# Optimization experiments

Measured on AMD Instinct MI355X. Metric: run time of the kernel, lower is better.

## Reference

```python
import jax, jax.numpy as jnp
import numpy as np
import math

NUM_HEADS = 32
KV_HEADS = 8
HEAD_DIM = 64
ROPE_BASE = 10000.0


def rotate_half(x):
    x1, x2 = jnp.split(x, 2, axis=-1)
    return jnp.concatenate([-x2, x1], axis=-1)


def rope_cos_sin(seq_len, head_dim, dtype):
    inv_freq = 1.0 / (ROPE_BASE ** (jnp.arange(0, head_dim, 2, dtype=jnp.float32) / head_dim))
    pos = jnp.arange(seq_len, dtype=jnp.float32)
    freqs = pos[:, None] * inv_freq[None, :]          # [S, D/2]
    emb = jnp.concatenate([freqs, freqs], axis=-1)    # [S, D]
    return jnp.cos(emb).astype(dtype), jnp.sin(emb).astype(dtype)


def setup_inputs() -> dict:
    key = jax.random.key(0)
    k1, k2, k3, k4, k5 = jax.random.split(key, 5)
    B, S, H = 2, 2048, 2048
    sc = 1.0 / math.sqrt(H)
    return {
        "hidden_states": jax.random.normal(k1, (B, S, H), jnp.float32),
        "Wq": jax.random.normal(k2, (H, H), jnp.float32) * sc,
        "Wk": jax.random.normal(k3, (KV_HEADS * HEAD_DIM, H), jnp.float32) * sc,
        "Wv": jax.random.normal(k4, (KV_HEADS * HEAD_DIM, H), jnp.float32) * sc,
        "Wo": jax.random.normal(k5, (H, H), jnp.float32) * sc,
    }


def reference(hidden_states, Wq, Wk, Wv, Wo):
    B, S, H = hidden_states.shape
    # projections (torch Linear: x @ W.T)
    q = (hidden_states @ Wq.T).reshape(B, S, NUM_HEADS, HEAD_DIM).transpose(0, 2, 1, 3)   # [B,Hq,S,D]
    k = (hidden_states @ Wk.T).reshape(B, S, KV_HEADS, HEAD_DIM).transpose(0, 2, 1, 3)    # [B,Hk,S,D]
    v = (hidden_states @ Wv.T).reshape(B, S, KV_HEADS, HEAD_DIM).transpose(0, 2, 1, 3)
    # inline RoPE
    cos, sin = rope_cos_sin(S, HEAD_DIM, q.dtype)   # [S,D], broadcasts over [B,h,S,D]
    q = q * cos + rotate_half(q) * sin
    k = k * cos + rotate_half(k) * sin
    # GQA: repeat KV heads
    rep = NUM_HEADS // KV_HEADS
    k = jnp.repeat(k, rep, axis=1)
    v = jnp.repeat(v, rep, axis=1)
    # scores + causal mask + softmax
    scores = jnp.einsum('bhqd,bhkd->bhqk', q, k) / math.sqrt(HEAD_DIM)
    causal = jnp.tril(jnp.ones((S, S), dtype=bool))
    scores = jnp.where(causal[None, None], scores, jnp.float32(-1e9))
    probs = jax.nn.softmax(scores.astype(jnp.float32), axis=-1).astype(q.dtype)
    ctx = jnp.einsum('bhqk,bhkd->bhqd', probs, v)
    ctx = ctx.transpose(0, 2, 1, 3).reshape(B, S, NUM_HEADS * HEAD_DIM)
    return ctx @ Wo.T
```

## Files before the change

### kernel.cpp

```cpp
#include <hip/hip_runtime.h>
#include <cstdint>
#include <cstddef>

typedef unsigned short ushort_t;
typedef __bf16 bf16x8 __attribute__((ext_vector_type(8)));
typedef ushort_t us8 __attribute__((ext_vector_type(8)));
typedef float f32x4 __attribute__((ext_vector_type(4)));

__device__ __forceinline__ ushort_t f2bf(float f) {
  union { float f; uint32_t u; } x; x.f = f;
  uint32_t r = (x.u + 0x7fffu + ((x.u >> 16) & 1u)) >> 16;
  return (ushort_t)r;
}
__device__ __forceinline__ float bf2f(ushort_t u) {
  union { uint32_t u; float f; } x; x.u = ((uint32_t)u) << 16;
  return x.f;
}
__device__ __forceinline__ float exp2_hw(float x) {
  float r;
  asm volatile("v_exp_f32 %0, %1\n\ts_nop 0" : "=v"(r) : "v"(x));
  return r;
}
__device__ __forceinline__ void gload_lds16(const void* g, void* l) {
  __builtin_amdgcn_global_load_lds(
      (const __attribute__((address_space(1))) void*)g,
      (__attribute__((address_space(3))) void*)l, 16, 0, 0);
}

__global__ void f32_to_bf16_kn(const float* __restrict__ in,
                               ushort_t* __restrict__ out, int n) {
  int i = (blockIdx.x * blockDim.x + threadIdx.x) * 4;
  if (i >= n) return;
  float4 v = *(const float4*)(in + i);
  ushort4 o;
  o.x = f2bf(v.x); o.y = f2bf(v.y); o.z = f2bf(v.z); o.w = f2bf(v.w);
  *(ushort4*)(out + i) = o;
}

__global__ void wconvert_kn(const float* __restrict__ Wq, const float* __restrict__ Wk,
                            const float* __restrict__ Wv, const float* __restrict__ Wo,
                            ushort_t* __restrict__ out) {
  int i = (blockIdx.x * blockDim.x + threadIdx.x) * 4;
  const float* src;
  int off;
  if (i < 4194304)      { src = Wq; off = i; }
  else if (i < 5242880) { src = Wk; off = i - 4194304; }
  else if (i < 6291456) { src = Wv; off = i - 5242880; }
  else                  { src = Wo; off = i - 6291456; }
  float4 v = *(const float4*)(src + off);
  ushort4 o;
  o.x = f2bf(v.x); o.y = f2bf(v.y); o.z = f2bf(v.z); o.w = f2bf(v.w);
  *(ushort4*)(out + i) = o;
}

template <int OUT_MODE>
__global__ __launch_bounds__(256, 2) void gemm_bt(
    const ushort_t* __restrict__ A, const ushort_t* __restrict__ Bw,
    void* __restrict__ Cout, void* __restrict__ Cout2, int M, int N, int K) {
  __shared__ __align__(16) ushort_t As[128 * 32];
  __shared__ __align__(16) ushort_t Bs[128 * 32];
  const int tid = threadIdx.x;
  const int lane = tid & 63;
  const int l15 = lane & 15, lq = lane >> 4;
  const int wid = tid >> 6;
  const int wm = (wid >> 1) * 64, wn = (wid & 1) * 64;
  const int m0 = blockIdx.x * 128, n0 = blockIdx.y * 128;

  const int seg = tid & 3;
  const int rrow = tid >> 2;
  const size_t aBase = (size_t)m0 * K + seg * 8;
  const size_t bBase = (size_t)n0 * K + seg * 8;
  const int ldsWaveBase = (tid & ~63) * 16;

  f32x4 acc[4][4] = {};
  const int nkt = K >> 5;
  for (int kt = 0; kt < nkt; ++kt) {
    const int kOff = kt * 32;
    __syncthreads();
#pragma unroll
    for (int j = 0; j < 2; ++j) {
      int row = j * 64 + rrow;
      gload_lds16(A + aBase + (size_t)row * K + kOff,
                  (char*)As + j * 4096 + ldsWaveBase);
      gload_lds16(Bw + bBase + (size_t)row * K + kOff,
                  (char*)Bs + j * 4096 + ldsWaveBase);
    }
    __syncthreads();
    bf16x8 af[4], bfv[4];
#pragma unroll
    for (int i = 0; i < 4; ++i) {
      af[i]  = *(const bf16x8*)(As + (wm + i * 16 + l15) * 32 + lq * 8);
      bfv[i] = *(const bf16x8*)(Bs + (wn + i * 16 + l15) * 32 + lq * 8);
    }
#pragma unroll
    for (int i = 0; i < 4; ++i)
#pragma unroll
      for (int j = 0; j < 4; ++j)
        acc[i][j] = __builtin_amdgcn_mfma_f32_16x16x32_bf16(af[i], bfv[j],
                                                            acc[i][j], 0, 0, 0);
  }

  if (OUT_MODE == 1) {
    float* C = (float*)Cout;
#pragma unroll
    for (int i = 0; i < 4; ++i) {
      int row = m0 + wm + i * 16 + lq * 4;
#pragma unroll
      for (int j = 0; j < 4; ++j) {
        int col = n0 + wn + j * 16 + l15;
#pragma unroll
        for (int r = 0; r < 4; ++r)
          C[(size_t)(row + r) * N + col] = acc[i][j][r];
      }
    }
  } else {
    ushort_t* qr = (ushort_t*)Cout;
    ushort_t* kvr = (ushort_t*)Cout2;
#pragma unroll
    for (int i = 0; i < 4; ++i) {
      int row = m0 + wm + i * 16 + lq * 4;
#pragma unroll
      for (int j = 0; j < 4; ++j) {
        int col = n0 + wn + j * 16 + l15;
#pragma unroll
        for (int r = 0; r < 4; ++r) {
          int rr = row + r;
          int b = rr >> 11, s = rr & 2047;
          if (col < 2048) {
            int h = col >> 6, d = col & 63;
            qr[((size_t)(b * 32 + h) * 2048 + s) * 64 + d] = f2bf(acc[i][j][r]);
          } else {
            int n2 = col - 2048;
            int head = n2 >> 6, d = n2 & 63;
            kvr[((size_t)(b * 16 + head) * 2048 + s) * 64 + d] = f2bf(acc[i][j][r]);
          }
        }
      }
    }
  }
}

__global__ void rope_kn(ushort_t* __restrict__ X, int nh, int batch_stride,
                        float scale, int total) {
  int idx = blockIdx.x * blockDim.x + threadIdx.x;
  if (idx >= total) return;
  int p = idx & 31;
  int t = idx >> 5;
  int s = t & 2047;
  int bh = t >> 11;
  int h = bh % nh, b = bh / nh;
  ushort_t* row = X + (size_t)b * batch_stride + ((size_t)h * 2048 + s) * 64;
  float a = (float)s * __builtin_exp2f((float)p * -0.4152410118609203f);
  float sn, c;
  __sincosf(a, &sn, &c);
  float x0 = bf2f(row[p]), x1 = bf2f(row[p + 32]);
  row[p]      = f2bf((x0 * c - x1 * sn) * scale);
  row[p + 32] = f2bf((x1 * c + x0 * sn) * scale);
}

#define PAD_K 72
#define PAD_P 76
__global__ __launch_bounds__(256, 4) void attn_kn(
    const ushort_t* __restrict__ Q, const ushort_t* __restrict__ KV,
    ushort_t* __restrict__ ctx) {
  __shared__ __align__(16) ushort_t Ks[64 * PAD_K];
  __shared__ __align__(16) ushort_t Vs[80 * PAD_K];
  __shared__ __align__(16) ushort_t Ps[4][16 * PAD_P];
  const int tid = threadIdx.x, wid = tid >> 6, lane = tid & 63;
  const int l15 = lane & 15, lq = lane >> 4;
  const int g = blockIdx.x;
  const int bh = g & 63;
  const int qidx = g >> 6;
  const int jq = qidx >> 2, sl = qidx & 3;
  const int qb = (jq & 1) ? (12 - 4 * jq + sl) : (15 - 4 * jq - sl);
  const int b = bh >> 5, h = bh & 31, hk = h >> 2;
  const int q0 = qb * 128;
  const int wq0 = q0 + wid * 32;

  for (int i = tid; i < 16 * PAD_K; i += 256)
    Vs[64 * PAD_K + i] = (i < PAD_K) ? (ushort_t)0x3F80 : (ushort_t)0;

  const ushort_t* Qb = Q + ((size_t)(b * 32 + h) * 2048) * 64;
  const ushort_t* Kb = KV + ((size_t)(b * 16 + hk) * 2048) * 64;
  const ushort_t* Vb = KV + ((size_t)(b * 16 + 8 + hk) * 2048) * 64;

  bf16x8 qf[2][2];
#pragma unroll
  for (int qg = 0; qg < 2; ++qg)
#pragma unroll
    for (int ks = 0; ks < 2; ++ks)
      qf[qg][ks] = *(const bf16x8*)(Qb + (size_t)(wq0 + qg * 16 + l15) * 64 +
                                    ks * 32 + lq * 8);

  f32x4 acc[2][5] = {};

  const int srow = tid >> 3, sseg = tid & 7;
  const int vd = tid & 63, vkg = tid >> 6;

  const int nkt = 2 * qb + 2;
  us8 kr0, kr1, vr0, vr1;
  {
    kr0 = *(const us8*)(Kb + (size_t)srow * 64 + sseg * 8);
    kr1 = *(const us8*)(Kb + (size_t)(32 + srow) * 64 + sseg * 8);
#pragma unroll
    for (int i = 0; i < 8; ++i) vr0[i] = Vb[(size_t)(vkg * 16 + i) * 64 + vd];
#pragma unroll
    for (int i = 0; i < 8; ++i) vr1[i] = Vb[(size_t)(vkg * 16 + 8 + i) * 64 + vd];
  }

  for (int kt = 0; kt < nkt; ++kt) {
    const int k0 = kt * 64;
    __syncthreads();
    *(us8*)(Ks + srow * PAD_K + sseg * 8) = kr0;
    *(us8*)(Ks + (32 + srow) * PAD_K + sseg * 8) = kr1;
    *(us8*)(Vs + vd * PAD_K + vkg * 16) = vr0;
    *(us8*)(Vs + vd * PAD_K + vkg * 16 + 8) = vr1;
    if (kt + 1 < nkt) {
      const int k1 = k0 + 64;
      kr0 = *(const us8*)(Kb + (size_t)(k1 + srow) * 64 + sseg * 8);
      kr1 = *(const us8*)(Kb + (size_t)(k1 + 32 + srow) * 64 + sseg * 8);
#pragma unroll
      for (int i = 0; i < 8; ++i)
        vr0[i] = Vb[(size_t)(k1 + vkg * 16 + i) * 64 + vd];
#pragma unroll
      for (int i = 0; i < 8; ++i)
        vr1[i] = Vb[(size_t)(k1 + vkg * 16 + 8 + i) * 64 + vd];
    }
    __syncthreads();

    if (k0 > wq0 + 31) continue;

#pragma unroll
    for (int qg = 0; qg < 2; ++qg) {
      const int rq0 = wq0 + qg * 16;
      f32x4 sf[4] = {};
      __builtin_amdgcn_s_setprio(1);
#pragma unroll
      for (int j = 0; j < 4; ++j)
#pragma unroll
        for (int ks = 0; ks < 2; ++ks)
          sf[j] = __builtin_amdgcn_mfma_f32_16x16x32_bf16(
              qf[qg][ks],
              *(const bf16x8*)(Ks + (j * 16 + l15) * PAD_K + ks * 32 + lq * 8),
              sf[j], 0, 0, 0);
      __builtin_amdgcn_s_setprio(0);

      if (k0 + 63 > rq0) {
#pragma unroll
        for (int j = 0; j < 4; ++j) {
          int kg = k0 + j * 16 + l15;
#pragma unroll
          for (int r = 0; r < 4; ++r) {
            int qrow = rq0 + lq * 4 + r;
            float p = (kg > qrow) ? 0.0f : exp2_hw(sf[j][r]);
            Ps[wid][(lq * 4 + r) * PAD_P + j * 16 + l15] = f2bf(p);
          }
        }
      } else {
#pragma unroll
        for (int j = 0; j < 4; ++j)
#pragma unroll
          for (int r = 0; r < 4; ++r)
            Ps[wid][(lq * 4 + r) * PAD_P + j * 16 + l15] = f2bf(exp2_hw(sf[j][r]));
      }

      bf16x8 pa[2];
#pragma unroll
      for (int ks = 0; ks < 2; ++ks)
        pa[ks] = *(const bf16x8*)(Ps[wid] + l15 * PAD_P + ks * 32 + lq * 8);

      __builtin_amdgcn_s_setprio(1);
#pragma unroll
      for (int dj = 0; dj < 5; ++dj) {
#pragma unroll
        for (int ks = 0; ks < 2; ++ks)
          acc[qg][dj] = __builtin_amdgcn_mfma_f32_16x16x32_bf16(
              pa[ks],
              *(const bf16x8*)(Vs + (dj * 16 + l15) * PAD_K + ks * 32 + lq * 8),
              acc[qg][dj], 0, 0, 0);
      }
      __builtin_amdgcn_s_setprio(0);
    }
  }

#pragma unroll
  for (int qg = 0; qg < 2; ++qg) {
    float linv[4];
#pragma unroll
    for (int r = 0; r < 4; ++r)
      linv[r] = 1.0f / __shfl(acc[qg][4][r], lane & 48);
#pragma unroll
    for (int dj = 0; dj < 4; ++dj)
#pragma unroll
      for (int r = 0; r < 4; ++r) {
        int qrow = wq0 + qg * 16 + lq * 4 + r;
        ctx[((size_t)(b * 2048 + qrow)) * 2048 + h * 64 + dj * 16 + l15] =
            f2bf(acc[qg][dj][r] * linv[r]);
      }
  }
}

extern "C" void kernel_launch(void* const* d_in, const int* in_sizes, int n_in,
                              void* d_out, int out_size, void* d_ws, size_t ws_size,
                              hipStream_t stream) {
  const float* hs = (const float*)d_in[0];
  const float* Wq = (const float*)d_in[1];
  const float* Wk = (const float*)d_in[2];
  const float* Wv = (const float*)d_in[3];
  const float* Wo = (const float*)d_in[4];

  char* ws = (char*)d_ws;
  ushort_t* hb   = (ushort_t*)(ws);
  ushort_t* wqb  = (ushort_t*)(ws + 16777216);
  ushort_t* wob  = (ushort_t*)(ws + 29360128);
  ushort_t* qr   = (ushort_t*)(ws + 37748736);
  ushort_t* kvr  = (ushort_t*)(ws + 54525952);
  ushort_t* ctx  = hb;

  f32_to_bf16_kn<<<8192, 256, 0, stream>>>(hs, hb, 8388608);
  wconvert_kn<<<10240, 256, 0, stream>>>(Wq, Wk, Wv, Wo, wqb);

  gemm_bt<2><<<dim3(32, 24), 256, 0, stream>>>(hb, wqb, qr, kvr, 4096, 3072, 2048);

  rope_kn<<<16384, 256, 0, stream>>>(qr, 32, 32 * 2048 * 64, 0.18033688f, 4194304);
  rope_kn<<<4096,  256, 0, stream>>>(kvr, 8, 16 * 2048 * 64, 1.0f, 1048576);

  attn_kn<<<dim3(1024), 256, 0, stream>>>(qr, kvr, ctx);

  gemm_bt<1><<<dim3(32, 16), 256, 0, stream>>>(ctx, wob, d_out, nullptr, 4096, 2048, 2048);
}
```

Before: 320.0 us.

## Replace 128x128 GEMM with double-buffered 256x256 swizzled-LDS GEMM

Both projection GEMMs move from a 128x128 tile, 256-thread kernel with K-step 32 to a 256x256 tile, 512-thread kernel with K-step 64. The new kernel double-buffers LDS, prefetching the next K tile while the current one is computed, and uses an XOR swizzle on LDS slots to avoid bank conflicts. It also raises wave priority around the MFMA block. This is meant to increase data reuse per tile and hide global-load latency. The cost is 128KB of LDS per block and more accumulator registers, which limits occupancy, and grids as small as 128 blocks may underfill the 256 CUs.

```diff
diff --git a/kernel.cpp b/kernel.cpp
--- a/kernel.cpp
+++ b/kernel.cpp
@@ -54,85 +54,107 @@
 }
 
 template <int OUT_MODE>
-__global__ __launch_bounds__(256, 2) void gemm_bt(
+__global__ __launch_bounds__(512, 2) void gemm256(
     const ushort_t* __restrict__ A, const ushort_t* __restrict__ Bw,
     void* __restrict__ Cout, void* __restrict__ Cout2, int M, int N, int K) {
-  __shared__ __align__(16) ushort_t As[128 * 32];
-  __shared__ __align__(16) ushort_t Bs[128 * 32];
+  __shared__ __align__(16) ushort_t lds[2][2][256 * 64];
   const int tid = threadIdx.x;
   const int lane = tid & 63;
   const int l15 = lane & 15, lq = lane >> 4;
   const int wid = tid >> 6;
-  const int wm = (wid >> 1) * 64, wn = (wid & 1) * 64;
-  const int m0 = blockIdx.x * 128, n0 = blockIdx.y * 128;
-
-  const int seg = tid & 3;
-  const int rrow = tid >> 2;
-  const size_t aBase = (size_t)m0 * K + seg * 8;
-  const size_t bBase = (size_t)n0 * K + seg * 8;
-  const int ldsWaveBase = (tid & ~63) * 16;
-
-  f32x4 acc[4][4] = {};
-  const int nkt = K >> 5;
-  for (int kt = 0; kt < nkt; ++kt) {
-    const int kOff = kt * 32;
-    __syncthreads();
-#pragma unroll
-    for (int j = 0; j < 2; ++j) {
-      int row = j * 64 + rrow;
-      gload_lds16(A + aBase + (size_t)row * K + kOff,
-                  (char*)As + j * 4096 + ldsWaveBase);
-      gload_lds16(Bw + bBase + (size_t)row * K + kOff,
-                  (char*)Bs + j * 4096 + ldsWaveBase);
-    }
-    __syncthreads();
-    bf16x8 af[4], bfv[4];
-#pragma unroll
-    for (int i = 0; i < 4; ++i) {
-      af[i]  = *(const bf16x8*)(As + (wm + i * 16 + l15) * 32 + lq * 8);
-      bfv[i] = *(const bf16x8*)(Bs + (wn + i * 16 + l15) * 32 + lq * 8);
-    }
-#pragma unroll
-    for (int i = 0; i < 4; ++i)
-#pragma unroll
-      for (int j = 0; j < 4; ++j)
-        acc[i][j] = __builtin_amdgcn_mfma_f32_16x16x32_bf16(af[i], bfv[j],
-                                                            acc[i][j], 0, 0, 0);
-  }
+  const int wr = wid >> 2, wc = wid & 3;
+  const int m0 = blockIdx.x * 256, n0 = blockIdx.y * 256;
+
+  const int sslot = (tid & 7) ^ ((tid >> 3) & 7);
+  const int ldsWaveByte = wid * 1024;
+  const size_t aRowBase = (size_t)(m0 + (tid >> 3)) * K + sslot * 8;
+  const size_t bRowBase = (size_t)(n0 + (tid >> 3)) * K + sslot * 8;
+
+  f32x4 acc[8][4] = {};
+  const int nkt = K >> 6;
+
+  const int s7 = l15 & 7;
+  const int aRow0 = (wr * 128 + l15) * 128;
+  const int bRow0 = (wc * 64 + l15) * 128;
+  const int oslot = (lq ^ s7) << 4;
+
+#define STAGE256(t, buf)                                                      \
+  {                                                                           \
+    const int kOff_ = (t) * 64;                                               \
+    _Pragma("unroll") for (int c = 0; c < 4; ++c)                             \
+        gload_lds16(A + aRowBase + (size_t)c * 64 * K + kOff_,                \
+                    (char*)&lds[buf][0][0] + c * 8192 + ldsWaveByte);         \
+    _Pragma("unroll") for (int c = 0; c < 4; ++c)                             \
+        gload_lds16(Bw + bRowBase + (size_t)c * 64 * K + kOff_,               \
+                    (char*)&lds[buf][1][0] + c * 8192 + ldsWaveByte);         \
+  }
+
+  STAGE256(0, 0);
+  for (int t = 0; t < nkt; ++t) {
+    const int tn = (t + 1 < nkt) ? t + 1 : t;
+    STAGE256(tn, (t + 1) & 1);
+    asm volatile("s_waitcnt vmcnt(8)" ::: "memory");
+    __builtin_amdgcn_s_barrier();
+    __builtin_amdgcn_sched_barrier(0);
+    const ushort_t* As = &lds[t & 1][0][0];
+    const ushort_t* Bs = &lds[t & 1][1][0];
+#pragma unroll
+    for (int k2 = 0; k2 < 2; ++k2) {
+      bf16x8 af[8], bfv[4];
+      const int ob = oslot ^ (k2 << 6);
+#pragma unroll
+      for (int m = 0; m < 8; ++m)
+        af[m] = *(const bf16x8*)((const char*)As + (aRow0 + m * 2048 + ob));
+#pragma unroll
+      for (int n = 0; n < 4; ++n)
+        bfv[n] = *(const bf16x8*)((const char*)Bs + (bRow0 + n * 2048 + ob));
+      __builtin_amdgcn_s_setprio(1);
+#pragma unroll
+      for (int m = 0; m < 8; ++m)
+#pragma unroll
+        for (int n = 0; n < 4; ++n)
+          acc[m][n] = __builtin_amdgcn_mfma_f32_16x16x32_bf16(af[m], bfv[n],
+                                                              acc[m][n], 0, 0, 0);
+      __builtin_amdgcn_s_setprio(0);
+    }
+    __builtin_amdgcn_sched_barrier(0);
+    __builtin_amdgcn_s_barrier();
+  }
+#undef STAGE256
 
   if (OUT_MODE == 1) {
     float* C = (float*)Cout;
 #pragma unroll
-    for (int i = 0; i < 4; ++i) {
-      int row = m0 + wm + i * 16 + lq * 4;
-#pragma unroll
-      for (int j = 0; j < 4; ++j) {
-        int col = n0 + wn + j * 16 + l15;
+    for (int m = 0; m < 8; ++m) {
+      int row = m0 + wr * 128 + m * 16 + lq * 4;
+#pragma unroll
+      for (int n = 0; n < 4; ++n) {
+        int col = n0 + wc * 64 + n * 16 + l15;
 #pragma unroll
         for (int r = 0; r < 4; ++r)
-          C[(size_t)(row + r) * N + col] = acc[i][j][r];
+          C[(size_t)(row + r) * N + col] = acc[m][n][r];
       }
     }
   } else {
     ushort_t* qr = (ushort_t*)Cout;
     ushort_t* kvr = (ushort_t*)Cout2;
 #pragma unroll
-    for (int i = 0; i < 4; ++i) {
-      int row = m0 + wm + i * 16 + lq * 4;
-#pragma unroll
-      for (int j = 0; j < 4; ++j) {
-        int col = n0 + wn + j * 16 + l15;
+    for (int m = 0; m < 8; ++m) {
+      int row = m0 + wr * 128 + m * 16 + lq * 4;
+#pragma unroll
+      for (int n = 0; n < 4; ++n) {
+        int col = n0 + wc * 64 + n * 16 + l15;
 #pragma unroll
         for (int r = 0; r < 4; ++r) {
           int rr = row + r;
           int b = rr >> 11, s = rr & 2047;
           if (col < 2048) {
             int h = col >> 6, d = col & 63;
-            qr[((size_t)(b * 32 + h) * 2048 + s) * 64 + d] = f2bf(acc[i][j][r]);
+            qr[((size_t)(b * 32 + h) * 2048 + s) * 64 + d] = f2bf(acc[m][n][r]);
           } else {
             int n2 = col - 2048;
             int head = n2 >> 6, d = n2 & 63;
-            kvr[((size_t)(b * 16 + head) * 2048 + s) * 64 + d] = f2bf(acc[i][j][r]);
+            kvr[((size_t)(b * 16 + head) * 2048 + s) * 64 + d] = f2bf(acc[m][n][r]);
           }
         }
       }
@@ -320,12 +342,12 @@
   f32_to_bf16_kn<<<8192, 256, 0, stream>>>(hs, hb, 8388608);
   wconvert_kn<<<10240, 256, 0, stream>>>(Wq, Wk, Wv, Wo, wqb);
 
-  gemm_bt<2><<<dim3(32, 24), 256, 0, stream>>>(hb, wqb, qr, kvr, 4096, 3072, 2048);
+  gemm256<2><<<dim3(16, 12), 512, 0, stream>>>(hb, wqb, qr, kvr, 4096, 3072, 2048);
 
   rope_kn<<<16384, 256, 0, stream>>>(qr, 32, 32 * 2048 * 64, 0.18033688f, 4194304);
   rope_kn<<<4096,  256, 0, stream>>>(kvr, 8, 16 * 2048 * 64, 1.0f, 1048576);
 
   attn_kn<<<dim3(1024), 256, 0, stream>>>(qr, kvr, ctx);
 
-  gemm_bt<1><<<dim3(32, 16), 256, 0, stream>>>(ctx, wob, d_out, nullptr, 4096, 2048, 2048);
-}
+  gemm256<1><<<dim3(16, 8), 512, 0, stream>>>(ctx, wob, d_out, nullptr, 4096, 2048, 2048);
+}
```

Measured after the change: 330.5 us. 1.03x slower.
